# Kernel tuning notes

Hardware: AMD Instinct MI355X
Metric: run time of the kernel (lower is better)

The kernel has to match this reference:

```python
import jax, jax.numpy as jnp
import numpy as np

B, T, D, E, P = 64, 512, 512, 6, 96
H = 4; HD = D // H; FF = 2048; L = 2


def setup_inputs() -> dict:
    key = jax.random.key(0)
    ks = iter(jax.random.split(key, 48))
    r = lambda shape, s=0.02: jax.random.normal(next(ks), shape, jnp.float32) * s
    return dict(
        x_enc=jax.random.normal(next(ks), (B, T, E), jnp.float32),
        x_mark_enc=jax.random.normal(next(ks), (B, T, 4), jnp.float32),
        x_dec=jax.random.normal(next(ks), (B, P, E), jnp.float32),
        x_mark_dec=jax.random.normal(next(ks), (B, P, 4), jnp.float32),
        omega=jnp.array([0.01], jnp.float32),
        alpha=jnp.array([-2.0], jnp.float32),
        beta=jnp.array([1.0], jnp.float32),
        gp_w=r((P, 1)), gp_b=r((P,)),
        w_ih=r((4 * D, E)), w_hh=r((4 * D, D)), b_ih=r((4 * D,)), b_hh=r((4 * D,)),
        attn_in_w=r((L, 3 * D, D)), attn_in_b=r((L, 3 * D)),
        attn_out_w=r((L, D, D)), attn_out_b=r((L, D)),
        ln1_g=jnp.ones((L, D), jnp.float32), ln1_b=jnp.zeros((L, D), jnp.float32),
        ffn_w1=r((L, FF, D)), ffn_b1=r((L, FF)), ffn_w2=r((L, D, FF)), ffn_b2=r((L, D)),
        ln2_g=jnp.ones((L, D), jnp.float32), ln2_b=jnp.zeros((L, D), jnp.float32),
        rh_w=r((P, D)), rh_b=r((P,)),
        g1_w=r((D // 2, E + 1)), g1_b=r((D // 2,)),
        g2_w=r((P, D // 2)), g2_b=r((P,)),
    )


def _layer_norm(x, g, b, eps=1e-5):
    mu = x.mean(-1, keepdims=True)
    var = x.var(-1, keepdims=True)
    return (x - mu) / jnp.sqrt(var + eps) * g + b


def reference(x_enc, x_mark_enc, x_dec, x_mark_dec, omega, alpha, beta,
              gp_w, gp_b, w_ih, w_hh, b_ih, b_hh,
              attn_in_w, attn_in_b, attn_out_w, attn_out_b,
              ln1_g, ln1_b, ffn_w1, ffn_b1, ffn_w2, ffn_b2, ln2_g, ln2_b,
              rh_w, rh_b, g1_w, g1_b, g2_w, g2_b):
    d = w_hh.shape[1]
    b_sz = x_enc.shape[0]
    # --- Neural GARCH: h_t = omega + alpha*r_{t-1}^2 + beta*h_{t-1} ---
    returns = x_enc[:, :, -1]                       # [B, T]
    om = jax.nn.softplus(omega)[0]
    al = (jax.nn.sigmoid(alpha) * 0.2)[0]
    be = (jax.nn.sigmoid(beta) * 0.8)[0]
    h0 = jnp.var(returns, axis=1, ddof=1) + 1e-6    # torch.var is unbiased; [B]
    r2 = (returns[:, :-1] ** 2).T                   # [T-1, B]

    def gstep(h, r2t):
        hn = om + al * r2t + be * h
        return hn, hn

    _, hs = jax.lax.scan(gstep, h0, r2)
    vol = jnp.sqrt(jnp.concatenate([h0[None], hs], axis=0))  # [T, B]
    vol_last = vol[-1]                              # [B]
    garch_base = vol_last[:, None] @ gp_w.T + gp_b  # [B, P]

    # --- single-layer LSTM (PyTorch gate order i,f,g,o) ---
    def lstep(carry, x_t):
        h, c = carry
        gates = x_t @ w_ih.T + h @ w_hh.T + b_ih + b_hh
        i, f, g, o = jnp.split(gates, 4, axis=-1)
        c = jax.nn.sigmoid(f) * c + jax.nn.sigmoid(i) * jnp.tanh(g)
        h = jax.nn.sigmoid(o) * jnp.tanh(c)
        return (h, c), h

    init = (jnp.zeros((b_sz, d), x_enc.dtype), jnp.zeros((b_sz, d), x_enc.dtype))
    _, hseq = jax.lax.scan(lstep, init, x_enc.transpose(1, 0, 2))
    x = hseq.transpose(1, 0, 2)                     # [B, T, D]

    # --- 2-layer TransformerEncoder (post-norm, relu FFN, eval mode) ---
    n_layers, n_heads = attn_in_w.shape[0], H
    hd = d // n_heads
    for l in range(n_layers):
        qkv = x @ attn_in_w[l].T + attn_in_b[l]
        q, k, v = jnp.split(qkv, 3, axis=-1)
        q = q.reshape(b_sz, -1, n_heads, hd)
        k = k.reshape(b_sz, -1, n_heads, hd)
        v = v.reshape(b_sz, -1, n_heads, hd)
        scores = jnp.einsum('bqhd,bkhd->bhqk', q, k) / jnp.sqrt(jnp.asarray(hd, x.dtype))
        attn = jax.nn.softmax(scores, axis=-1)
        ctx = jnp.einsum('bhqk,bkhd->bqhd', attn, v).reshape(b_sz, -1, d)
        attn_out = ctx @ attn_out_w[l].T + attn_out_b[l]
        x = _layer_norm(x + attn_out, ln1_g[l], ln1_b[l])
        ff = jax.nn.relu(x @ ffn_w1[l].T + ffn_b1[l]) @ ffn_w2[l].T + ffn_b2[l]
        x = _layer_norm(x + ff, ln2_g[l], ln2_b[l])

    ai_residual = x[:, -1, :] @ rh_w.T + rh_b        # [B, P]

    # --- dynamic gate ---
    gate_in = jnp.concatenate([x_enc[:, -1, :], vol_last[:, None]], axis=1)
    gate = jax.nn.sigmoid(jax.nn.relu(gate_in @ g1_w.T + g1_b) @ g2_w.T + g2_b)

    final = garch_base + gate * ai_residual          # [B, P]
    return final[..., None]                          # [B, P, 1]
```

## Files before the change

### kernel.cpp

```cpp
#include <hip/hip_runtime.h>
#include <hip/hip_bf16.h>

#define BB 64
#define TT 512
#define DD 512
#define EE 6
#define PP 96
#define NHH 4
#define HDD 128
#define FFF 2048

typedef short bf16x8 __attribute__((ext_vector_type(8)));
typedef float f32x4 __attribute__((ext_vector_type(4)));

__device__ __forceinline__ float bf2f(unsigned short u) {
    unsigned int x = ((unsigned int)u) << 16;
    return __uint_as_float(x);
}
__device__ __forceinline__ unsigned short f2bf(float f) {
    __hip_bfloat16 h = __float2bfloat16(f);
    return *reinterpret_cast<unsigned short*>(&h);
}

__device__ __forceinline__ void gload_lds16(const unsigned short* g, unsigned short* l)
{
    __builtin_amdgcn_global_load_lds(
        (const __attribute__((address_space(1))) unsigned int*)g,
        (__attribute__((address_space(3))) unsigned int*)l, 16, 0, 0);
}

template<bool TRANSW, bool BIAS, bool RELU, bool OUTBF16>
__global__ __launch_bounds__(256) void gemm_bt(
    const unsigned short* __restrict__ A, int lda, long long aB, long long aH,
    const unsigned short* __restrict__ W, int ldw, long long wB, long long wH,
    const float* __restrict__ bias,
    void* __restrict__ Cv, int ldc, long long cB, long long cH,
    int K, int Hdiv, float alpha)
{
    __shared__ unsigned short As[128 * 32];
    __shared__ unsigned short Ws[128 * 32];
    int t = threadIdx.x;
    int z = blockIdx.z;
    int zb = z / Hdiv, zh = z - zb * Hdiv;
    long long aOff = (long long)zb * aB + (long long)zh * aH;
    long long wOff = (long long)zb * wB + (long long)zh * wH;
    long long cOff = (long long)zb * cB + (long long)zh * cH;
    int m0 = blockIdx.x * 128, n0 = blockIdx.y * 128;

    int wave = t >> 6, lane = t & 63;

    int srow = wave * 16 + (lane >> 2);
    int scol = (lane & 3) * 8;
    const unsigned short* AgL = A + aOff + (long long)(m0 + srow) * lda + scol;
    const unsigned short* AgH = A + aOff + (long long)(m0 + 64 + srow) * lda + scol;
    unsigned short* AsL = &As[(wave * 16) * 32];
    unsigned short* AsH = &As[(64 + wave * 16) * 32];
    const unsigned short* WgL = W + wOff + (long long)(n0 + srow) * ldw + scol;
    const unsigned short* WgH = W + wOff + (long long)(n0 + 64 + srow) * ldw + scol;
    unsigned short* WsL = &Ws[(wave * 16) * 32];
    unsigned short* WsH = &Ws[(64 + wave * 16) * 32];

    int wk = t >> 3, wn = (t & 7) * 16;
    const unsigned short* WgT = W + wOff + n0 + wn;

    int wm = (wave & 1) * 64, wn2 = (wave >> 1) * 64;
    int lrow = lane & 15, quad = lane >> 4;

    f32x4 acc[4][4];
    #pragma unroll
    for (int i = 0; i < 4; i++)
        #pragma unroll
        for (int j = 0; j < 4; j++)
            acc[i][j] = (f32x4){0.f, 0.f, 0.f, 0.f};

    for (int k0 = 0; k0 < K; k0 += 32) {
        __syncthreads();
        gload_lds16(AgL + k0, AsL);
        gload_lds16(AgH + k0, AsH);
        if (!TRANSW) {
            gload_lds16(WgL + k0, WsL);
            gload_lds16(WgH + k0, WsH);
        } else {
            const unsigned short* p = WgT + (long long)(k0 + wk) * ldw;
            uint4 w0 = *(const uint4*)(p);
            uint4 w1 = *(const uint4*)(p + 8);
            const unsigned short* s0 = (const unsigned short*)&w0;
            const unsigned short* s1 = (const unsigned short*)&w1;
            #pragma unroll
            for (int j = 0; j < 8; j++) Ws[(wn + j) * 32 + wk] = s0[j];
            #pragma unroll
            for (int j = 0; j < 8; j++) Ws[(wn + 8 + j) * 32 + wk] = s1[j];
        }
        __syncthreads();
        bf16x8 af[4], bf[4];
        #pragma unroll
        for (int i = 0; i < 4; i++)
            af[i] = *(const bf16x8*)&As[(wm + i * 16 + lrow) * 32 + quad * 8];
        #pragma unroll
        for (int j = 0; j < 4; j++)
            bf[j] = *(const bf16x8*)&Ws[(wn2 + j * 16 + lrow) * 32 + quad * 8];
        #pragma unroll
        for (int i = 0; i < 4; i++)
            #pragma unroll
            for (int j = 0; j < 4; j++)
                acc[i][j] = __builtin_amdgcn_mfma_f32_16x16x32_bf16(af[i], bf[j], acc[i][j], 0, 0, 0);
    }

    #pragma unroll
    for (int i = 0; i < 4; i++) {
        #pragma unroll
        for (int j = 0; j < 4; j++) {
            #pragma unroll
            for (int r = 0; r < 4; r++) {
                int row = m0 + wm + i * 16 + quad * 4 + r;
                int col = n0 + wn2 + j * 16 + lrow;
                float v = acc[i][j][r] * alpha;
                if (BIAS) v += bias[col];
                if (RELU) v = fmaxf(v, 0.f);
                long long idx = cOff + (long long)row * ldc + col;
                if (OUTBF16) ((unsigned short*)Cv)[idx] = f2bf(v);
                else         ((float*)Cv)[idx] = v;
            }
        }
    }
}

__global__ void cvt_k(const float* __restrict__ in, unsigned short* __restrict__ out, int n)
{
    int i = blockIdx.x * 256 + threadIdx.x;
    int stride = gridDim.x * 256;
    for (; i < n; i += stride) out[i] = f2bf(in[i]);
}

__global__ __launch_bounds__(64) void garch_k(
    const float* __restrict__ xe, const float* __restrict__ omega,
    const float* __restrict__ alpha, const float* __restrict__ beta,
    float* __restrict__ vol)
{
    int b = threadIdx.x;
    float sm = 0.f, sq = 0.f;
    for (int t2 = 0; t2 < TT; t2++) {
        float r = xe[((long long)b * TT + t2) * EE + 5];
        sm += r; sq += r * r;
    }
    float mean = sm / 512.f;
    float var = (sq - 512.f * mean * mean) / 511.f;
    float h = var + 1e-6f;
    float om = log1pf(expf(omega[0]));
    float al = 0.2f / (1.f + expf(-alpha[0]));
    float be = 0.8f / (1.f + expf(-beta[0]));
    for (int t2 = 0; t2 < TT - 1; t2++) {
        float r = xe[((long long)b * TT + t2) * EE + 5];
        h = om + al * r * r + be * h;
    }
    vol[b] = sqrtf(h);
}

__global__ __launch_bounds__(512, 1) void lstm_wreg3_k(
    const float* __restrict__ xe, const float* __restrict__ w_hh,
    const float* __restrict__ w_ih, const float* __restrict__ b_ih,
    const float* __restrict__ b_hh,
    float* __restrict__ h0, float* __restrict__ h1,
    float* __restrict__ xT,
    unsigned* __restrict__ root)
{
    __shared__ float hs[8][544];
    __shared__ float xs[8][8];
    __shared__ float wsx[16][4][6];
    __shared__ float bsx[16][4];

    int blk = blockIdx.x;
    int dgG = blk >> 3;
    int bG  = blk & 7;
    int tid = threadIdx.x;
    int i   = tid >> 5;
    int ks  = tid & 31;
    int D   = dgG * 16 + i;
    int lane = tid & 63;
    int go  = lane & 32;

    float w[4][16];
    #pragma unroll
    for (int g = 0; g < 4; g++) {
        const float* wr = w_hh + ((long long)(g * 512 + D)) * 512 + ks * 16;
        #pragma unroll
        for (int jj = 0; jj < 4; jj++) {
            float4 v4 = *(const float4*)(wr + jj * 4);
            w[g][jj * 4 + 0] = v4.x; w[g][jj * 4 + 1] = v4.y;
            w[g][jj * 4 + 2] = v4.z; w[g][jj * 4 + 3] = v4.w;
        }
    }
    for (int idx = tid; idx < 16 * 4 * 6; idx += 512) {
        int i2 = idx / 24, g = (idx / 6) % 4, e = idx % 6;
        wsx[i2][g][e] = w_ih[((g * 512) + (dgG * 16 + i2)) * 6 + e];
    }
    if (tid < 64) {
        int i2 = tid >> 2, g = tid & 3;
        int D2 = dgG * 16 + i2;
        bsx[i2][g] = b_ih[g * 512 + D2] + b_hh[g * 512 + D2];
    }
    float c = 0.f;

    for (int t = 0; t < TT; t++) {
        const float* hin  = (t & 1) ? h1 : h0;
        float*       hout = (t & 1) ? h0 : h1;

        float hv[8];
        #pragma unroll
        for (int jj = 0; jj < 8; jj++) {
            int flat = jj * 512 + tid;
            int row = flat >> 9, k = flat & 511;
            hv[jj] = __hip_atomic_load(&hin[(bG * 8 + row) * 512 + k],
                                       __ATOMIC_RELAXED,
                                       __HIP_MEMORY_SCOPE_AGENT);
        }
        if (tid < 64 && (tid & 7) < 6) {
            int b = tid >> 3, e = tid & 7;
            xs[b][e] = xe[((long long)(bG * 8 + b) * TT + t) * EE + e];
        }
        #pragma unroll
        for (int jj = 0; jj < 8; jj++) {
            int flat = jj * 512 + tid;
            int row = flat >> 9, k = flat & 511;
            hs[row][k + 2 * (k >> 5)] = hv[jj];
        }
        __syncthreads();

        float v[32];
        #pragma unroll
        for (int s = 0; s < 32; s++) v[s] = 0.f;

        int kbase = ks * 16 + 2 * (ks >> 1);
        #pragma unroll
        for (int jj = 0; jj < 8; jj++) {
            float2 hb2[8];
            #pragma unroll
            for (int b = 0; b < 8; b++)
                hb2[b] = *(const float2*)&hs[b][kbase + jj * 2];
            #pragma unroll
            for (int g = 0; g < 4; g++)
                #pragma unroll
                for (int b = 0; b < 8; b++) {
                    v[g * 8 + b] += w[g][jj * 2]     * hb2[b].x;
                    v[g * 8 + b] += w[g][jj * 2 + 1] * hb2[b].y;
                }
        }

        float t16[16];
        #pragma unroll
        for (int j = 0; j < 16; j++) {
            float send = (ks & 16) ? v[j] : v[j + 16];
            float recv = __shfl_xor(send, 16);
            t16[j] = ((ks & 16) ? v[j + 16] : v[j]) + recv;
        }
        float t8[8];
        #pragma unroll
        for (int j = 0; j < 8; j++) {
            float send = (ks & 8) ? t16[j] : t16[j + 8];
            float recv = __shfl_xor(send, 8);
            t8[j] = ((ks & 8) ? t16[j + 8] : t16[j]) + recv;
        }
        float t4[4];
        #pragma unroll
        for (int j = 0; j < 4; j++) {
            float send = (ks & 4) ? t8[j] : t8[j + 4];
            float recv = __shfl_xor(send, 4);
            t4[j] = ((ks & 4) ? t8[j + 4] : t8[j]) + recv;
        }
        float t2[2];
        #pragma unroll
        for (int j = 0; j < 2; j++) {
            float send = (ks & 2) ? t4[j] : t4[j + 2];
            float recv = __shfl_xor(send, 2);
            t2[j] = ((ks & 2) ? t4[j + 2] : t4[j]) + recv;
        }
        float red;
        {
            float send = (ks & 1) ? t2[0] : t2[1];
            float recv = __shfl_xor(send, 1);
            red = ((ks & 1) ? t2[1] : t2[0]) + recv;
        }

        int gg_ = ks >> 3, bb_ = ks & 7;
        float x0 = xs[bb_][0], x1 = xs[bb_][1], x2 = xs[bb_][2];
        float x3 = xs[bb_][3], x4 = xs[bb_][4], x5 = xs[bb_][5];
        float p = red + x0 * wsx[i][gg_][0] + x1 * wsx[i][gg_][1]
                      + x2 * wsx[i][gg_][2] + x3 * wsx[i][gg_][3]
                      + x4 * wsx[i][gg_][4] + x5 * wsx[i][gg_][5]
                      + bsx[i][gg_];
        float sg = 1.f / (1.f + __expf(-p));
        float th = tanhf(p);
        float act = (gg_ == 2) ? th : sg;

        float ai = __shfl(act, go + 0  + bb_);
        float af = __shfl(act, go + 8  + bb_);
        float ag = __shfl(act, go + 16 + bb_);
        float ao = __shfl(act, go + 24 + bb_);

        if (ks < 8) {
            int b = ks;
            c = af * c + ai * ag;
            float hn = ao * tanhf(c);
            __hip_atomic_store(&hout[(bG * 8 + b) * 512 + D], hn,
                               __ATOMIC_RELAXED, __HIP_MEMORY_SCOPE_AGENT);
            xT[((long long)t * 512 + D) * 64 + (bG * 8 + b)] = hn;
            asm volatile("s_waitcnt vmcnt(0)" ::: "memory");
        }
        __syncthreads();

        if (t < TT - 1) {
            if (tid == 0) {
                __hip_atomic_fetch_add(&root[t * 8 + bG], 1u,
                    __ATOMIC_RELAXED, __HIP_MEMORY_SCOPE_AGENT);
                unsigned tries = 0;
                while (__hip_atomic_load(&root[t * 8 + bG], __ATOMIC_RELAXED,
                                         __HIP_MEMORY_SCOPE_AGENT) < 32u) {
                    __builtin_amdgcn_s_sleep(2);
                    if (++tries > 100000000u) break;
                }
            }
            __syncthreads();
        }
    }
}

__global__ __launch_bounds__(256) void transpose_k(
    const float* __restrict__ xT, unsigned short* __restrict__ XB_)
{
    __shared__ float tile[64][65];
    int dc = blockIdx.x, t = blockIdx.y;
    int tid = threadIdx.x;
    int bcol = tid & 63, grp = tid >> 6;
    #pragma unroll
    for (int j = 0; j < 16; j++) {
        int i = grp * 16 + j;
        tile[i][bcol] = xT[((long long)t * 512 + dc * 64 + i) * 64 + bcol];
    }
    __syncthreads();
    #pragma unroll
    for (int j = 0; j < 16; j++) {
        int brow = grp * 16 + j;
        float v = tile[bcol][brow];
        long long idx = ((long long)brow * TT + t) * DD + dc * 64 + bcol;
        XB_[idx] = f2bf(v);
    }
}

__global__ __launch_bounds__(256) void softmax_k(unsigned short* __restrict__ S)
{
    long long row = (long long)blockIdx.x * 4 + (threadIdx.x >> 6);
    int lane = threadIdx.x & 63;
    unsigned short* p = S + row * 512 + lane * 8;
    uint4 raw = *(const uint4*)p;
    unsigned short* u = (unsigned short*)&raw;
    float v[8];
    float m = -1e30f;
    #pragma unroll
    for (int j = 0; j < 8; j++) { v[j] = bf2f(u[j]); m = fmaxf(m, v[j]); }
    #pragma unroll
    for (int off = 1; off < 64; off <<= 1) m = fmaxf(m, __shfl_xor(m, off));
    float s = 0.f;
    #pragma unroll
    for (int j = 0; j < 8; j++) { v[j] = __expf(v[j] - m); s += v[j]; }
    #pragma unroll
    for (int off = 1; off < 64; off <<= 1) s += __shfl_xor(s, off);
    float inv = 1.f / s;
    unsigned int pk[4];
    #pragma unroll
    for (int j = 0; j < 4; j++)
        pk[j] = (unsigned int)f2bf(v[2 * j] * inv) | ((unsigned int)f2bf(v[2 * j + 1] * inv) << 16);
    *(uint4*)p = make_uint4(pk[0], pk[1], pk[2], pk[3]);
}

__global__ __launch_bounds__(256) void ln_k(
    unsigned short* XB_, const float* __restrict__ Y_,
    const float* __restrict__ g, const float* __restrict__ b2)
{
    long long row = (long long)blockIdx.x * 4 + (threadIdx.x >> 6);
    int lane = threadIdx.x & 63;
    long long base = row * 512 + lane * 8;
    float s[8];
    {
        uint4 xr = *(const uint4*)&XB_[base];
        const unsigned short* xu = (const unsigned short*)&xr;
        float4 y0 = *(const float4*)&Y_[base];
        float4 y1 = *(const float4*)&Y_[base + 4];
        s[0] = bf2f(xu[0]) + y0.x; s[1] = bf2f(xu[1]) + y0.y;
        s[2] = bf2f(xu[2]) + y0.z; s[3] = bf2f(xu[3]) + y0.w;
        s[4] = bf2f(xu[4]) + y1.x; s[5] = bf2f(xu[5]) + y1.y;
        s[6] = bf2f(xu[6]) + y1.z; s[7] = bf2f(xu[7]) + y1.w;
    }
    float sm = 0.f, sq = 0.f;
    #pragma unroll
    for (int j = 0; j < 8; j++) { sm += s[j]; sq += s[j] * s[j]; }
    #pragma unroll
    for (int off = 1; off < 64; off <<= 1) {
        sm += __shfl_xor(sm, off);
        sq += __shfl_xor(sq, off);
    }
    float mean = sm * (1.f / 512.f);
    float var = sq * (1.f / 512.f) - mean * mean;
    float rstd = rsqrtf(var + 1e-5f);
    int col = lane * 8;
    float o[8];
    #pragma unroll
    for (int j = 0; j < 8; j++) o[j] = (s[j] - mean) * rstd * g[col + j] + b2[col + j];
    unsigned int pk[4];
    #pragma unroll
    for (int j = 0; j < 4; j++)
        pk[j] = (unsigned int)f2bf(o[2 * j]) | ((unsigned int)f2bf(o[2 * j + 1]) << 16);
    *(uint4*)&XB_[base] = make_uint4(pk[0], pk[1], pk[2], pk[3]);
}

__global__ __launch_bounds__(128) void head_k(
    const unsigned short* __restrict__ XB_, const float* __restrict__ xe,
    const float* __restrict__ vol,
    const float* __restrict__ rh_w, const float* __restrict__ rh_b,
    const float* __restrict__ g1_w, const float* __restrict__ g1_b,
    const float* __restrict__ g2_w, const float* __restrict__ g2_b,
    const float* __restrict__ gp_w, const float* __restrict__ gp_b,
    float* __restrict__ out)
{
    int b = blockIdx.x, t = threadIdx.x;
    __shared__ float xl[512];
    __shared__ float hid[256];
    for (int j = t; j < 512; j += 128)
        xl[j] = bf2f(XB_[((long long)b * TT + (TT - 1)) * DD + j]);
    float gin[7];
    #pragma unroll
    for (int e = 0; e < 6; e++) gin[e] = xe[((long long)b * TT + (TT - 1)) * EE + e];
    gin[6] = vol[b];
    for (int j = t; j < 256; j += 128) {
        float s = g1_b[j];
        #pragma unroll
        for (int e = 0; e < 7; e++) s += g1_w[j * 7 + e] * gin[e];
        hid[j] = fmaxf(s, 0.f);
    }
    __syncthreads();
    for (int p = t; p < 96; p += 128) {
        float ai = rh_b[p];
        for (int j = 0; j < 512; j++) ai += xl[j] * rh_w[p * 512 + j];
        float gs = g2_b[p];
        for (int j = 0; j < 256; j++) gs += hid[j] * g2_w[p * 256 + j];
        float gate = 1.f / (1.f + expf(-gs));
        out[b * PP + p] = vol[b] * gp_w[p] + gp_b[p] + gate * ai;
    }
}

extern "C" void kernel_launch(void* const* d_in, const int* in_sizes, int n_in,
                              void* d_out, int out_size, void* d_ws, size_t ws_size,
                              hipStream_t stream)
{
    const float* x_enc      = (const float*)d_in[0];
    const float* omega      = (const float*)d_in[4];
    const float* alpha      = (const float*)d_in[5];
    const float* beta       = (const float*)d_in[6];
    const float* gp_w       = (const float*)d_in[7];
    const float* gp_b       = (const float*)d_in[8];
    const float* w_ih       = (const float*)d_in[9];
    const float* w_hh       = (const float*)d_in[10];
    const float* b_ih       = (const float*)d_in[11];
    const float* b_hh       = (const float*)d_in[12];
    const float* attn_in_w  = (const float*)d_in[13];
    const float* attn_in_b  = (const float*)d_in[14];
    const float* attn_out_w = (const float*)d_in[15];
    const float* attn_out_b = (const float*)d_in[16];
    const float* ln1_g      = (const float*)d_in[17];
    const float* ln1_b      = (const float*)d_in[18];
    const float* ffn_w1     = (const float*)d_in[19];
    const float* ffn_b1     = (const float*)d_in[20];
    const float* ffn_w2     = (const float*)d_in[21];
    const float* ffn_b2     = (const float*)d_in[22];
    const float* ln2_g      = (const float*)d_in[23];
    const float* ln2_b      = (const float*)d_in[24];
    const float* rh_w       = (const float*)d_in[25];
    const float* rh_b       = (const float*)d_in[26];
    const float* g1_w       = (const float*)d_in[27];
    const float* g1_b       = (const float*)d_in[28];
    const float* g2_w       = (const float*)d_in[29];
    const float* g2_b       = (const float*)d_in[30];

    char* ws = (char*)d_ws;
    unsigned short* XB   = (unsigned short*)(ws + 0);
    float*          Y    = (float*)(ws + 33554432LL);
    float*          XT   = Y;
    unsigned short* QKVc = (unsigned short*)(ws + 100663296LL);
    unsigned short* SCc  = (unsigned short*)(ws + 113246208LL);
    unsigned short* CTXc = (unsigned short*)(ws + 130023424LL);
    unsigned short* HIDc = (unsigned short*)(ws + 100663296LL);
    unsigned short* WATI = (unsigned short*)(ws + 134217728LL);
    unsigned short* WATO = WATI + 1572864;
    unsigned short* WF1  = WATI + 2097152;
    unsigned short* WF2  = WATI + 4194304;
    float*          HT0  = (float*)(ws + 146800640LL);
    float*          HT1  = (float*)(ws + 146931712LL);
    unsigned*       ROOT = (unsigned*)(ws + 147062784LL);
    float*          VOL  = (float*)(ws + 147193856LL);

    hipMemsetAsync(HT0, 0, 131072, stream);
    hipMemsetAsync(ROOT, 0, 16384, stream);

    cvt_k<<<2048, 256, 0, stream>>>(attn_in_w,  WATI, 1572864);
    cvt_k<<<1024, 256, 0, stream>>>(attn_out_w, WATO, 524288);
    cvt_k<<<2048, 256, 0, stream>>>(ffn_w1,     WF1,  2097152);
    cvt_k<<<2048, 256, 0, stream>>>(ffn_w2,     WF2,  2097152);

    garch_k<<<1, 64, 0, stream>>>(x_enc, omega, alpha, beta, VOL);

    lstm_wreg3_k<<<256, 512, 0, stream>>>(x_enc, w_hh, w_ih, b_ih, b_hh,
                                          HT0, HT1, XT, ROOT);

    transpose_k<<<dim3(8, 512, 1), 256, 0, stream>>>(XT, XB);

    for (int l = 0; l < 2; l++) {
        for (int c = 0; c < 8; c++) {
            long long rowOff = (long long)c * 8 * 512;
            gemm_bt<false, true, false, true><<<dim3(32, 12, 1), 256, 0, stream>>>(
                XB + rowOff * 512, 512, 0, 0,
                WATI + l * 786432, 512, 0, 0, attn_in_b + l * 1536,
                QKVc, 1536, 0, 0, 512, 1, 1.0f);
            gemm_bt<false, false, false, true><<<dim3(4, 4, 32), 256, 0, stream>>>(
                QKVc, 1536, 786432LL, 128LL, QKVc + 512, 1536, 786432LL, 128LL, nullptr,
                SCc, 512, 1048576LL, 262144LL, 128, 4, 0.088388347648318447f);
            softmax_k<<<4096, 256, 0, stream>>>(SCc);
            gemm_bt<true, false, false, true><<<dim3(4, 1, 32), 256, 0, stream>>>(
                SCc, 512, 1048576LL, 262144LL, QKVc + 1024, 1536, 786432LL, 128LL, nullptr,
                CTXc, 512, 262144LL, 128LL, 512, 4, 1.0f);
            gemm_bt<false, true, false, false><<<dim3(32, 4, 1), 256, 0, stream>>>(
                CTXc, 512, 0, 0, WATO + l * 262144, 512, 0, 0, attn_out_b + l * 512,
                Y + rowOff * 512, 512, 0, 0, 512, 1, 1.0f);
        }
        ln_k<<<8192, 256, 0, stream>>>(XB, Y, ln1_g + l * 512, ln1_b + l * 512);

        for (int mc = 0; mc < 4; mc++) {
            long long rowOff = (long long)mc * 8192;
            gemm_bt<false, true, true, true><<<dim3(64, 16, 1), 256, 0, stream>>>(
                XB + rowOff * 512, 512, 0, 0,
                WF1 + l * 1048576, 512, 0, 0, ffn_b1 + l * 2048,
                HIDc, 2048, 0, 0, 512, 1, 1.0f);
            gemm_bt<false, true, false, false><<<dim3(64, 4, 1), 256, 0, stream>>>(
                HIDc, 2048, 0, 0, WF2 + l * 1048576, 2048, 0, 0, ffn_b2 + l * 512,
                Y + rowOff * 512, 512, 0, 0, 2048, 1, 1.0f);
        }
        ln_k<<<8192, 256, 0, stream>>>(XB, Y, ln2_g + l * 512, ln2_b + l * 512);
    }

    head_k<<<64, 128, 0, stream>>>(XB, x_enc, VOL, rh_w, rh_b,
                                   g1_w, g1_b, g2_w, g2_b, gp_w, gp_b,
                                   (float*)d_out);
}
```

Baseline: 4.264 ms.

## Store residual outputs in bf16, double attention chunk size, parallelize GARCH

The attention and FFN output projections now write bf16 instead of fp32, and layer norm reads bf16 residuals, which halves that intermediate traffic. The attention loop processes 16 batches per chunk instead of 8, so it issues fewer, larger launches. The context output is written back into the Q slot of the QKV buffer, removing the separate CTX buffer. The GARCH kernel splits the statistics pass across 8 threads per batch and keeps r² in shared memory for the serial recurrence. The trade-off is precision lost by rounding the projection outputs to bf16 before the residual add.

Result: faster. 3.805 ms (-10.8%).

```diff
diff --git a/kernel.cpp b/kernel.cpp
--- a/kernel.cpp
+++ b/kernel.cpp
@@ -132,28 +132,37 @@
     for (; i < n; i += stride) out[i] = f2bf(in[i]);
 }
 
-__global__ __launch_bounds__(64) void garch_k(
+__global__ __launch_bounds__(512) void garch2_k(
     const float* __restrict__ xe, const float* __restrict__ omega,
     const float* __restrict__ alpha, const float* __restrict__ beta,
     float* __restrict__ vol)
 {
-    int b = threadIdx.x;
+    __shared__ float r2s[64][513];
+    int tid = threadIdx.x;
+    int b = tid >> 3, j = tid & 7;
     float sm = 0.f, sq = 0.f;
-    for (int t2 = 0; t2 < TT; t2++) {
-        float r = xe[((long long)b * TT + t2) * EE + 5];
+    for (int t = j; t < TT; t += 8) {
+        float r = xe[((long long)b * TT + t) * EE + 5];
+        r2s[b][t] = r * r;
         sm += r; sq += r * r;
     }
-    float mean = sm / 512.f;
-    float var = (sq - 512.f * mean * mean) / 511.f;
-    float h = var + 1e-6f;
-    float om = log1pf(expf(omega[0]));
-    float al = 0.2f / (1.f + expf(-alpha[0]));
-    float be = 0.8f / (1.f + expf(-beta[0]));
-    for (int t2 = 0; t2 < TT - 1; t2++) {
-        float r = xe[((long long)b * TT + t2) * EE + 5];
-        h = om + al * r * r + be * h;
-    }
-    vol[b] = sqrtf(h);
+    #pragma unroll
+    for (int off = 1; off < 8; off <<= 1) {
+        sm += __shfl_xor(sm, off);
+        sq += __shfl_xor(sq, off);
+    }
+    __syncthreads();
+    if (j == 0) {
+        float mean = sm / 512.f;
+        float var = (sq - 512.f * mean * mean) / 511.f;
+        float h = var + 1e-6f;
+        float om = log1pf(expf(omega[0]));
+        float al = 0.2f / (1.f + expf(-alpha[0]));
+        float be = 0.8f / (1.f + expf(-beta[0]));
+        for (int t = 0; t < TT - 1; t++)
+            h = om + al * r2s[b][t] + be * h;
+        vol[b] = sqrtf(h);
+    }
 }
 
 __global__ __launch_bounds__(512, 1) void lstm_wreg3_k(
@@ -373,7 +382,7 @@
 }
 
 __global__ __launch_bounds__(256) void ln_k(
-    unsigned short* XB_, const float* __restrict__ Y_,
+    unsigned short* XB_, const unsigned short* __restrict__ Y_,
     const float* __restrict__ g, const float* __restrict__ b2)
 {
     long long row = (long long)blockIdx.x * 4 + (threadIdx.x >> 6);
@@ -382,13 +391,11 @@
     float s[8];
     {
         uint4 xr = *(const uint4*)&XB_[base];
+        uint4 yr = *(const uint4*)&Y_[base];
         const unsigned short* xu = (const unsigned short*)&xr;
-        float4 y0 = *(const float4*)&Y_[base];
-        float4 y1 = *(const float4*)&Y_[base + 4];
-        s[0] = bf2f(xu[0]) + y0.x; s[1] = bf2f(xu[1]) + y0.y;
-        s[2] = bf2f(xu[2]) + y0.z; s[3] = bf2f(xu[3]) + y0.w;
-        s[4] = bf2f(xu[4]) + y1.x; s[5] = bf2f(xu[5]) + y1.y;
-        s[6] = bf2f(xu[6]) + y1.z; s[7] = bf2f(xu[7]) + y1.w;
+        const unsigned short* yu = (const unsigned short*)&yr;
+        #pragma unroll
+        for (int j = 0; j < 8; j++) s[j] = bf2f(xu[j]) + bf2f(yu[j]);
     }
     float sm = 0.f, sq = 0.f;
     #pragma unroll
@@ -482,16 +489,15 @@
 
     char* ws = (char*)d_ws;
     unsigned short* XB   = (unsigned short*)(ws + 0);
-    float*          Y    = (float*)(ws + 33554432LL);
-    float*          XT   = Y;
-    unsigned short* QKVc = (unsigned short*)(ws + 100663296LL);
-    unsigned short* SCc  = (unsigned short*)(ws + 113246208LL);
-    unsigned short* CTXc = (unsigned short*)(ws + 130023424LL);
-    unsigned short* HIDc = (unsigned short*)(ws + 100663296LL);
+    unsigned short* YB   = (unsigned short*)(ws + 33554432LL);
+    float*          XT   = (float*)(ws + 67108864LL);
+    unsigned short* QKVc = (unsigned short*)(ws + 67108864LL);
+    unsigned short* SCc  = (unsigned short*)(ws + 67108864LL + 25165824LL);
     unsigned short* WATI = (unsigned short*)(ws + 134217728LL);
     unsigned short* WATO = WATI + 1572864;
     unsigned short* WF1  = WATI + 2097152;
     unsigned short* WF2  = WATI + 4194304;
+    unsigned short* HIDc = QKVc;
     float*          HT0  = (float*)(ws + 146800640LL);
     float*          HT1  = (float*)(ws + 146931712LL);
     unsigned*       ROOT = (unsigned*)(ws + 147062784LL);
@@ -505,7 +511,7 @@
     cvt_k<<<2048, 256, 0, stream>>>(ffn_w1,     WF1,  2097152);
     cvt_k<<<2048, 256, 0, stream>>>(ffn_w2,     WF2,  2097152);
 
-    garch_k<<<1, 64, 0, stream>>>(x_enc, omega, alpha, beta, VOL);
+    garch2_k<<<1, 512, 0, stream>>>(x_enc, omega, alpha, beta, VOL);
 
     lstm_wreg3_k<<<256, 512, 0, stream>>>(x_enc, w_hh, w_ih, b_ih, b_hh,
                                           HT0, HT1, XT, ROOT);
@@ -513,24 +519,24 @@
     transpose_k<<<dim3(8, 512, 1), 256, 0, stream>>>(XT, XB);
 
     for (int l = 0; l < 2; l++) {
-        for (int c = 0; c < 8; c++) {
-            long long rowOff = (long long)c * 8 * 512;
-            gemm_bt<false, true, false, true><<<dim3(32, 12, 1), 256, 0, stream>>>(
+        for (int c = 0; c < 4; c++) {
+            long long rowOff = (long long)c * 16 * 512;
+            gemm_bt<false, true, false, true><<<dim3(64, 12, 1), 256, 0, stream>>>(
                 XB + rowOff * 512, 512, 0, 0,
                 WATI + l * 786432, 512, 0, 0, attn_in_b + l * 1536,
                 QKVc, 1536, 0, 0, 512, 1, 1.0f);
-            gemm_bt<false, false, false, true><<<dim3(4, 4, 32), 256, 0, stream>>>(
+            gemm_bt<false, false, false, true><<<dim3(4, 4, 64), 256, 0, stream>>>(
                 QKVc, 1536, 786432LL, 128LL, QKVc + 512, 1536, 786432LL, 128LL, nullptr,
                 SCc, 512, 1048576LL, 262144LL, 128, 4, 0.088388347648318447f);
-            softmax_k<<<4096, 256, 0, stream>>>(SCc);
-            gemm_bt<true, false, false, true><<<dim3(4, 1, 32), 256, 0, stream>>>(
+            softmax_k<<<8192, 256, 0, stream>>>(SCc);
+            gemm_bt<true, false, false, true><<<dim3(4, 1, 64), 256, 0, stream>>>(
                 SCc, 512, 1048576LL, 262144LL, QKVc + 1024, 1536, 786432LL, 128LL, nullptr,
-                CTXc, 512, 262144LL, 128LL, 512, 4, 1.0f);
-            gemm_bt<false, true, false, false><<<dim3(32, 4, 1), 256, 0, stream>>>(
-                CTXc, 512, 0, 0, WATO + l * 262144, 512, 0, 0, attn_out_b + l * 512,
-                Y + rowOff * 512, 512, 0, 0, 512, 1, 1.0f);
-        }
-        ln_k<<<8192, 256, 0, stream>>>(XB, Y, ln1_g + l * 512, ln1_b + l * 512);
+                QKVc, 1536, 786432LL, 128LL, 512, 4, 1.0f);
+            gemm_bt<false, true, false, true><<<dim3(64, 4, 1), 256, 0, stream>>>(
+                QKVc, 1536, 0, 0, WATO + l * 262144, 512, 0, 0, attn_out_b + l * 512,
+                YB + rowOff * 512, 512, 0, 0, 512, 1, 1.0f);
+        }
+        ln_k<<<8192, 256, 0, stream>>>(XB, YB, ln1_g + l * 512, ln1_b + l * 512);
 
         for (int mc = 0; mc < 4; mc++) {
             long long rowOff = (long long)mc * 8192;
@@ -538,11 +544,11 @@
                 XB + rowOff * 512, 512, 0, 0,
                 WF1 + l * 1048576, 512, 0, 0, ffn_b1 + l * 2048,
                 HIDc, 2048, 0, 0, 512, 1, 1.0f);
-            gemm_bt<false, true, false, false><<<dim3(64, 4, 1), 256, 0, stream>>>(
+            gemm_bt<false, true, false, true><<<dim3(64, 4, 1), 256, 0, stream>>>(
                 HIDc, 2048, 0, 0, WF2 + l * 1048576, 2048, 0, 0, ffn_b2 + l * 512,
-                Y + rowOff * 512, 512, 0, 0, 2048, 1, 1.0f);
-        }
-        ln_k<<<8192, 256, 0, stream>>>(XB, Y, ln2_g + l * 512, ln2_b + l * 512);
+                YB + rowOff * 512, 512, 0, 0, 2048, 1, 1.0f);
+        }
+        ln_k<<<8192, 256, 0, stream>>>(XB, YB, ln2_g + l * 512, ln2_b + l * 512);
     }
 
     head_k<<<64, 128, 0, stream>>>(XB, x_enc, VOL, rh_w, rh_b,
```
